# Performance work log

Measured on AMD Instinct MI355X. Metric: run time of the kernel, lower is better.

Reference implementation:

```python
import jax, jax.numpy as jnp
import numpy as np

RANK = 16
LN_EPS = 1e-5


def _layer_norm(x, eps=LN_EPS):
    mu = jnp.mean(x, axis=-1, keepdims=True)
    var = jnp.var(x, axis=-1, keepdims=True)
    return (x - mu) / jnp.sqrt(var + eps)


def setup_inputs() -> dict:
    key = jax.random.key(0)
    ks = jax.random.split(key, 8)
    B, S, D, M, R = 32, 4096, 160, 16, RANK
    query = jax.random.normal(ks[0], (B, S, D), dtype=jnp.float32)
    interface = jax.random.normal(ks[1], (B, S, D), dtype=jnp.float32)
    memory = jax.random.normal(ks[2], (B, M, D), dtype=jnp.float32)
    sd = 1.0 / np.sqrt(D)
    sr = 1.0 / np.sqrt(R)
    # torch nn.Linear weights: [out_features, in_features]
    W_read_key = jax.random.uniform(ks[3], (R, D), minval=-sd, maxval=sd, dtype=jnp.float32)
    W_read_value = jax.random.uniform(ks[4], (D, R), minval=-sr, maxval=sr, dtype=jnp.float32)
    W_write_key = jax.random.uniform(ks[5], (R, D), minval=-sd, maxval=sd, dtype=jnp.float32)
    W_write_erase = jax.random.uniform(ks[6], (D, R), minval=-sr, maxval=sr, dtype=jnp.float32)
    W_write_add = jax.random.uniform(ks[7], (D, R), minval=-sr, maxval=sr, dtype=jnp.float32)
    return {
        "query": query,
        "interface": interface,
        "memory": memory,
        "W_read_key": W_read_key,
        "W_read_value": W_read_value,
        "W_write_key": W_write_key,
        "W_write_erase": W_write_erase,
        "W_write_add": W_write_add,
    }


def reference(query, interface, memory, W_read_key, W_read_value,
              W_write_key, W_write_erase, W_write_add):
    R = RANK
    # ---- read ----
    q_proj = jnp.einsum('bsd,rd->bsr', query, W_read_key)          # [B,S,R]
    mem_proj = memory[..., :R]                                      # [B,M,R]
    scores = jnp.einsum('bsr,bmr->bsm', q_proj, mem_proj) / jnp.sqrt(jnp.float32(R))
    attn = jax.nn.softmax(scores, axis=-1)                          # [B,S,M]
    content = jnp.einsum('bsm,bmd->bsd', attn, memory)              # [B,S,D]
    read_out = jnp.einsum('bsr,dr->bsd', content[..., :R], W_read_value)
    # ---- write ----
    i_mean = jnp.mean(interface, axis=1)                            # [B,D]
    i_proj = jnp.einsum('bd,rd->br', i_mean, W_write_key)           # [B,R]
    erase = jax.nn.sigmoid(jnp.einsum('br,dr->bd', i_proj, W_write_erase))[:, None, :]
    add = jnp.einsum('br,dr->bd', i_proj, W_write_add)[:, None, :]
    new_memory = _layer_norm(memory * (1.0 - erase) + add)          # [B,M,D]
    return read_out, new_memory
```

## Files before the change

### kernel.cpp

```cpp
#include <hip/hip_runtime.h>
#include <hip/hip_bf16.h>
#include <math.h>

#define NB 32
#define NS 4096
#define ND 160
#define ND4 40
#define NM 16
#define NR 16
#define TPB 64
#define NCB (NS / TPB)

typedef float  f32x4  __attribute__((ext_vector_type(4)));
typedef short  bf16x8 __attribute__((ext_vector_type(8)));
typedef unsigned int u32x4 __attribute__((ext_vector_type(4)));

__device__ __forceinline__ unsigned short f2bf(float f) {
    union { __hip_bfloat16 b; unsigned short s; } x;
    x.b = __float2bfloat16(f);
    return x.s;
}
__device__ __forceinline__ unsigned bfpair(float lo, float hi) {
    return ((unsigned)f2bf(hi) << 16) | (unsigned)f2bf(lo);
}
__device__ __forceinline__ bf16x8 asfrag(u32x4 u) {
    union { u32x4 u; bf16x8 h; } x; x.u = u; return x.h;
}

__global__ __launch_bounds__(256) void ulm_read_kernel(
    const float* __restrict__ query,
    const float* __restrict__ iface,
    const float* __restrict__ memory,
    const float* __restrict__ Wrk,
    const float* __restrict__ Wrv,
    float* __restrict__ read_out,
    float* __restrict__ ipart)
{
    __shared__ unsigned sG[4][160];
    __shared__ unsigned sPm[4][160];
    __shared__ unsigned sH[4][160];
    __shared__ float4 sIred[4 * ND4];

    const int t = threadIdx.x;
    const int chunk = blockIdx.x;
    const int b = blockIdx.y;
    const int s0 = chunk * TPB;
    const int w  = t >> 6;
    const int l  = t & 63;
    const int lr = l & 15;
    const int lg = l >> 4;
    const bool lo2 = (lg < 2);

    const size_t base = (size_t)b * NS * ND;
    const int tok = s0 + w * 16 + lr;

    const float4* q4 = reinterpret_cast<const float4*>(query + base);
    float4 qr[10];
#pragma unroll
    for (int kb = 0; kb < 5; ++kb) {
        qr[2*kb]   = q4[(size_t)tok * ND4 + lg * 2 + kb * 8];
        qr[2*kb+1] = q4[(size_t)tok * ND4 + lg * 2 + kb * 8 + 1];
    }

    const float4* wk4 = reinterpret_cast<const float4*>(Wrk);
    u32x4 wf[5];
#pragma unroll
    for (int kb = 0; kb < 5; ++kb) {
        float4 a = wk4[lr * ND4 + kb * 8 + lg * 2];
        float4 c = wk4[lr * ND4 + kb * 8 + lg * 2 + 1];
        wf[kb] = (u32x4){bfpair(a.x, a.y), bfpair(a.z, a.w),
                         bfpair(c.x, c.y), bfpair(c.z, c.w)};
    }

    f32x4 G = {0.f, 0.f, 0.f, 0.f};
#pragma unroll
    for (int kb = 0; kb < 5; ++kb) {
        u32x4 qf = (u32x4){bfpair(qr[2*kb].x,   qr[2*kb].y),
                           bfpair(qr[2*kb].z,   qr[2*kb].w),
                           bfpair(qr[2*kb+1].x, qr[2*kb+1].y),
                           bfpair(qr[2*kb+1].z, qr[2*kb+1].w)};
        G = __builtin_amdgcn_mfma_f32_16x16x32_bf16(asfrag(wf[kb]), asfrag(qf), G, 0, 0, 0);
    }

    unsigned* gl = &sG[w][0];
    gl[lr * 10 + lg * 2 + 0] = bfpair(G[0], G[1]);
    gl[lr * 10 + lg * 2 + 1] = bfpair(G[2], G[3]);
    asm volatile("s_waitcnt lgkmcnt(0)" ::: "memory");
    int gb = lo2 ? (lr * 10 + lg * 4) : 0;
    u32x4 gf = (u32x4){gl[gb], gl[gb + 1], gl[gb + 2], gl[gb + 3]};

    u32x4 mf = (u32x4){0u, 0u, 0u, 0u};
    if (lo2) {
        const float4* m4 = reinterpret_cast<const float4*>(
            memory + ((size_t)b * NM + lr) * ND + lg * 8);
        float4 a = m4[0], c = m4[1];
        mf = (u32x4){bfpair(0.25f * a.x, 0.25f * a.y),
                     bfpair(0.25f * a.z, 0.25f * a.w),
                     bfpair(0.25f * c.x, 0.25f * c.y),
                     bfpair(0.25f * c.z, 0.25f * c.w)};
    }
    f32x4 S = {0.f, 0.f, 0.f, 0.f};
    S = __builtin_amdgcn_mfma_f32_16x16x32_bf16(asfrag(mf), asfrag(gf), S, 0, 0, 0);

    const float4* i4 = reinterpret_cast<const float4*>(iface + base);
    const int l8 = l & 7, g8 = l >> 3;
    const int itok = s0 + w * 16 + g8 * 2;
    float4 iv[10];
#pragma unroll
    for (int j = 0; j < 2; ++j)
#pragma unroll
        for (int k = 0; k < 5; ++k)
            iv[j * 5 + k] = i4[(size_t)(itok + j) * ND4 + l8 + 8 * k];

    float mx = fmaxf(fmaxf(S[0], S[1]), fmaxf(S[2], S[3]));
    mx = fmaxf(mx, __shfl_xor(mx, 16));
    mx = fmaxf(mx, __shfl_xor(mx, 32));
    float e0 = __expf(S[0] - mx), e1 = __expf(S[1] - mx);
    float e2 = __expf(S[2] - mx), e3 = __expf(S[3] - mx);
    float sm = e0 + e1 + e2 + e3;
    sm += __shfl_xor(sm, 16);
    sm += __shfl_xor(sm, 32);
    float inv = 1.f / sm;
    e0 *= inv; e1 *= inv; e2 *= inv; e3 *= inv;

    unsigned* pl = &sPm[w][0];
    pl[lr * 10 + lg * 2 + 0] = bfpair(e0, e1);
    pl[lr * 10 + lg * 2 + 1] = bfpair(e2, e3);
    asm volatile("s_waitcnt lgkmcnt(0)" ::: "memory");
    int pb = lo2 ? (lr * 10 + lg * 4) : 0;
    u32x4 pf = (u32x4){pl[pb], pl[pb + 1], pl[pb + 2], pl[pb + 3]};

    u32x4 mtf = (u32x4){0u, 0u, 0u, 0u};
    if (lo2) {
        float f0 = memory[((size_t)b * NM + lg * 8 + 0) * ND + lr];
        float f1 = memory[((size_t)b * NM + lg * 8 + 1) * ND + lr];
        float f2 = memory[((size_t)b * NM + lg * 8 + 2) * ND + lr];
        float f3 = memory[((size_t)b * NM + lg * 8 + 3) * ND + lr];
        float f4 = memory[((size_t)b * NM + lg * 8 + 4) * ND + lr];
        float f5 = memory[((size_t)b * NM + lg * 8 + 5) * ND + lr];
        float f6 = memory[((size_t)b * NM + lg * 8 + 6) * ND + lr];
        float f7 = memory[((size_t)b * NM + lg * 8 + 7) * ND + lr];
        mtf = (u32x4){bfpair(f0, f1), bfpair(f2, f3),
                      bfpair(f4, f5), bfpair(f6, f7)};
    }
    f32x4 H = {0.f, 0.f, 0.f, 0.f};
    H = __builtin_amdgcn_mfma_f32_16x16x32_bf16(asfrag(mtf), asfrag(pf), H, 0, 0, 0);

    unsigned* hl = &sH[w][0];
    hl[lr * 10 + lg * 2 + 0] = bfpair(H[0], H[1]);
    hl[lr * 10 + lg * 2 + 1] = bfpair(H[2], H[3]);
    asm volatile("s_waitcnt lgkmcnt(0)" ::: "memory");
    int hb = lo2 ? (lr * 10 + lg * 4) : 0;
    u32x4 hf = (u32x4){hl[hb], hl[hb + 1], hl[hb + 2], hl[hb + 3]};

    const float4* wv4 = reinterpret_cast<const float4*>(Wrv);
    float4* out4 = reinterpret_cast<float4*>(read_out + base);
#pragma unroll
    for (int db = 0; db < 10; ++db) {
        u32x4 vf = (u32x4){0u, 0u, 0u, 0u};
        if (lo2) {
            float4 a = wv4[(db * 16 + lr) * 4 + lg * 2];
            float4 c = wv4[(db * 16 + lr) * 4 + lg * 2 + 1];
            vf = (u32x4){bfpair(a.x, a.y), bfpair(a.z, a.w),
                         bfpair(c.x, c.y), bfpair(c.z, c.w)};
        }
        f32x4 C = {0.f, 0.f, 0.f, 0.f};
        C = __builtin_amdgcn_mfma_f32_16x16x32_bf16(asfrag(vf), asfrag(hf), C, 0, 0, 0);
        out4[(size_t)tok * ND4 + db * 4 + lg] = make_float4(C[0], C[1], C[2], C[3]);
    }

#pragma unroll
    for (int k = 0; k < 5; ++k) {
        float x = iv[k].x + iv[5 + k].x, y = iv[k].y + iv[5 + k].y;
        float z = iv[k].z + iv[5 + k].z, u = iv[k].w + iv[5 + k].w;
#pragma unroll
        for (int off = 8; off <= 32; off <<= 1) {
            x += __shfl_xor(x, off); y += __shfl_xor(y, off);
            z += __shfl_xor(z, off); u += __shfl_xor(u, off);
        }
        if (l < 8) sIred[w * ND4 + k * 8 + l8] = make_float4(x, y, z, u);
    }
    __syncthreads();
    if (t < ND4) {
        float4 a0 = sIred[t], a1 = sIred[ND4 + t];
        float4 a2 = sIred[2 * ND4 + t], a3 = sIred[3 * ND4 + t];
        float4 tot = make_float4(a0.x + a1.x + a2.x + a3.x,
                                 a0.y + a1.y + a2.y + a3.y,
                                 a0.z + a1.z + a2.z + a3.z,
                                 a0.w + a1.w + a2.w + a3.w);
        reinterpret_cast<float4*>(ipart + ((size_t)(b * NCB + chunk)) * ND)[t] = tot;
    }
}

__global__ __launch_bounds__(256) void ulm_write_kernel(
    const float* __restrict__ memory,
    const float* __restrict__ Wwk,
    const float* __restrict__ Wwe,
    const float* __restrict__ Wwa,
    const float* __restrict__ ipart,
    float* __restrict__ new_mem)
{
    __shared__ float sIm[ND];
    __shared__ float sIp[NR];
    __shared__ float sOmE[ND];
    __shared__ float sAdd[ND];

    const int b = blockIdx.x;
    const int t = threadIdx.x;

    if (t < ND) {
        float acc = 0.f;
#pragma unroll 8
        for (int c = 0; c < NCB; ++c)
            acc += ipart[((size_t)(b * NCB + c)) * ND + t];
        sIm[t] = acc * (1.0f / NS);
    }
    __syncthreads();

    if (t < NR) {
        float acc = 0.f;
        for (int d = 0; d < ND; ++d) acc += sIm[d] * Wwk[t * ND + d];
        sIp[t] = acc;
    }
    __syncthreads();

    if (t < ND) {
        float e = 0.f, a = 0.f;
#pragma unroll
        for (int r = 0; r < NR; ++r) {
            float ip = sIp[r];
            e += ip * Wwe[t * NR + r];
            a += ip * Wwa[t * NR + r];
        }
        sOmE[t] = 1.0f - 1.0f / (1.0f + __expf(-e));
        sAdd[t] = a;
    }
    __syncthreads();

    const int wave = t >> 6, lane = t & 63;
    for (int m = wave; m < NM; m += 4) {
        const float* mrow = memory + ((size_t)b * NM + m) * ND;
        float v0 = mrow[lane] * sOmE[lane] + sAdd[lane];
        float v1 = mrow[lane + 64] * sOmE[lane + 64] + sAdd[lane + 64];
        float v2 = 0.f;
        const bool has2 = lane < 32;
        if (has2) v2 = mrow[lane + 128] * sOmE[lane + 128] + sAdd[lane + 128];
        float s  = v0 + v1 + v2;
        float sq = v0 * v0 + v1 * v1 + v2 * v2;
#pragma unroll
        for (int off = 32; off; off >>= 1) {
            s  += __shfl_xor(s, off);
            sq += __shfl_xor(sq, off);
        }
        float mu   = s * (1.0f / ND);
        float var  = sq * (1.0f / ND) - mu * mu;
        float rstd = rsqrtf(var + 1e-5f);
        float* orow = new_mem + ((size_t)b * NM + m) * ND;
        orow[lane]      = (v0 - mu) * rstd;
        orow[lane + 64] = (v1 - mu) * rstd;
        if (has2) orow[lane + 128] = (v2 - mu) * rstd;
    }
}

extern "C" void kernel_launch(void* const* d_in, const int* in_sizes, int n_in,
                              void* d_out, int out_size, void* d_ws, size_t ws_size,
                              hipStream_t stream) {
    const float* query  = (const float*)d_in[0];
    const float* iface  = (const float*)d_in[1];
    const float* memory = (const float*)d_in[2];
    const float* Wrk    = (const float*)d_in[3];
    const float* Wrv    = (const float*)d_in[4];
    const float* Wwk    = (const float*)d_in[5];
    const float* Wwe    = (const float*)d_in[6];
    const float* Wwa    = (const float*)d_in[7];

    float* read_out = (float*)d_out;
    float* new_mem  = (float*)d_out + (size_t)NB * NS * ND;
    float* ipart    = (float*)d_ws;

    dim3 grid1(NCB, NB);
    ulm_read_kernel<<<grid1, 256, 0, stream>>>(query, iface, memory, Wrk, Wrv,
                                               read_out, ipart);
    ulm_write_kernel<<<NB, 256, 0, stream>>>(memory, Wwk, Wwe, Wwa, ipart, new_mem);
}
```

Measured before the change: 58.19 us.

## Move interface mean reduction into dedicated extra blocks of the read kernel

The interface column-sum moves out of every read block and into 8 extra blocks per batch. Each of these blocks accumulates over 512 tokens and writes one partial, so the write kernel now sums 8 partials instead of 64. This removes the per-block interface loads, shuffle reduction and __syncthreads from the attention path. The cost is load imbalance: the 8 reduction blocks each stream far more data than a read block and may finish last, lengthening the tail.

Result: faster. 55.76 us (-4.2%).

```diff
diff --git a/kernel.cpp b/kernel.cpp
--- a/kernel.cpp
+++ b/kernel.cpp
@@ -10,6 +10,8 @@
 #define NR 16
 #define TPB 64
 #define NCB (NS / TPB)
+#define NIC 8
+#define ITOK (NS / NIC)
 
 typedef float  f32x4  __attribute__((ext_vector_type(4)));
 typedef short  bf16x8 __attribute__((ext_vector_type(8)));
@@ -44,14 +46,54 @@
     const int t = threadIdx.x;
     const int chunk = blockIdx.x;
     const int b = blockIdx.y;
-    const int s0 = chunk * TPB;
     const int w  = t >> 6;
     const int l  = t & 63;
+    const size_t base = (size_t)b * NS * ND;
+
+    if (chunk >= NCB) {
+        const int ic = chunk - NCB;
+        const float4* i4 = reinterpret_cast<const float4*>(iface + base);
+        const int l8 = l & 7, g8 = l >> 3;
+        float4 ia[5];
+#pragma unroll
+        for (int k = 0; k < 5; ++k) ia[k] = make_float4(0.f, 0.f, 0.f, 0.f);
+#pragma unroll 4
+        for (int p = 0; p < 16; ++p) {
+            size_t tk = (size_t)(ic * ITOK + p * 32 + w * 8 + g8);
+#pragma unroll
+            for (int k = 0; k < 5; ++k) {
+                float4 v = i4[tk * ND4 + l8 + 8 * k];
+                ia[k].x += v.x; ia[k].y += v.y;
+                ia[k].z += v.z; ia[k].w += v.w;
+            }
+        }
+#pragma unroll
+        for (int k = 0; k < 5; ++k) {
+            float x = ia[k].x, y = ia[k].y, z = ia[k].z, u = ia[k].w;
+#pragma unroll
+            for (int off = 8; off <= 32; off <<= 1) {
+                x += __shfl_xor(x, off); y += __shfl_xor(y, off);
+                z += __shfl_xor(z, off); u += __shfl_xor(u, off);
+            }
+            if (l < 8) sIred[w * ND4 + k * 8 + l8] = make_float4(x, y, z, u);
+        }
+        __syncthreads();
+        if (t < ND4) {
+            float4 a0 = sIred[t], a1 = sIred[ND4 + t];
+            float4 a2 = sIred[2 * ND4 + t], a3 = sIred[3 * ND4 + t];
+            float4 tot = make_float4(a0.x + a1.x + a2.x + a3.x,
+                                     a0.y + a1.y + a2.y + a3.y,
+                                     a0.z + a1.z + a2.z + a3.z,
+                                     a0.w + a1.w + a2.w + a3.w);
+            reinterpret_cast<float4*>(ipart + ((size_t)(b * NIC + ic)) * ND)[t] = tot;
+        }
+        return;
+    }
+
+    const int s0 = chunk * TPB;
     const int lr = l & 15;
     const int lg = l >> 4;
     const bool lo2 = (lg < 2);
-
-    const size_t base = (size_t)b * NS * ND;
     const int tok = s0 + w * 16 + lr;
 
     const float4* q4 = reinterpret_cast<const float4*>(query + base);
@@ -101,16 +143,6 @@
     }
     f32x4 S = {0.f, 0.f, 0.f, 0.f};
     S = __builtin_amdgcn_mfma_f32_16x16x32_bf16(asfrag(mf), asfrag(gf), S, 0, 0, 0);
-
-    const float4* i4 = reinterpret_cast<const float4*>(iface + base);
-    const int l8 = l & 7, g8 = l >> 3;
-    const int itok = s0 + w * 16 + g8 * 2;
-    float4 iv[10];
-#pragma unroll
-    for (int j = 0; j < 2; ++j)
-#pragma unroll
-        for (int k = 0; k < 5; ++k)
-            iv[j * 5 + k] = i4[(size_t)(itok + j) * ND4 + l8 + 8 * k];
 
     float mx = fmaxf(fmaxf(S[0], S[1]), fmaxf(S[2], S[3]));
     mx = fmaxf(mx, __shfl_xor(mx, 16));
@@ -168,28 +200,6 @@
         C = __builtin_amdgcn_mfma_f32_16x16x32_bf16(asfrag(vf), asfrag(hf), C, 0, 0, 0);
         out4[(size_t)tok * ND4 + db * 4 + lg] = make_float4(C[0], C[1], C[2], C[3]);
     }
-
-#pragma unroll
-    for (int k = 0; k < 5; ++k) {
-        float x = iv[k].x + iv[5 + k].x, y = iv[k].y + iv[5 + k].y;
-        float z = iv[k].z + iv[5 + k].z, u = iv[k].w + iv[5 + k].w;
-#pragma unroll
-        for (int off = 8; off <= 32; off <<= 1) {
-            x += __shfl_xor(x, off); y += __shfl_xor(y, off);
-            z += __shfl_xor(z, off); u += __shfl_xor(u, off);
-        }
-        if (l < 8) sIred[w * ND4 + k * 8 + l8] = make_float4(x, y, z, u);
-    }
-    __syncthreads();
-    if (t < ND4) {
-        float4 a0 = sIred[t], a1 = sIred[ND4 + t];
-        float4 a2 = sIred[2 * ND4 + t], a3 = sIred[3 * ND4 + t];
-        float4 tot = make_float4(a0.x + a1.x + a2.x + a3.x,
-                                 a0.y + a1.y + a2.y + a3.y,
-                                 a0.z + a1.z + a2.z + a3.z,
-                                 a0.w + a1.w + a2.w + a3.w);
-        reinterpret_cast<float4*>(ipart + ((size_t)(b * NCB + chunk)) * ND)[t] = tot;
-    }
 }
 
 __global__ __launch_bounds__(256) void ulm_write_kernel(
@@ -210,9 +220,9 @@
 
     if (t < ND) {
         float acc = 0.f;
-#pragma unroll 8
-        for (int c = 0; c < NCB; ++c)
-            acc += ipart[((size_t)(b * NCB + c)) * ND + t];
+#pragma unroll
+        for (int c = 0; c < NIC; ++c)
+            acc += ipart[((size_t)(b * NIC + c)) * ND + t];
         sIm[t] = acc * (1.0f / NS);
     }
     __syncthreads();
@@ -278,7 +288,7 @@
     float* new_mem  = (float*)d_out + (size_t)NB * NS * ND;
     float* ipart    = (float*)d_ws;
 
-    dim3 grid1(NCB, NB);
+    dim3 grid1(NCB + NIC, NB);
     ulm_read_kernel<<<grid1, 256, 0, stream>>>(query, iface, memory, Wrk, Wrv,
                                                read_out, ipart);
     ulm_write_kernel<<<NB, 256, 0, stream>>>(memory, Wwk, Wwe, Wwa, ipart, new_mem);
```
